# Kernel tuning notes

Measured on AMD Instinct MI355X. Metric: run time of the kernel, lower is better.

Reference implementation:

```python
import jax, jax.numpy as jnp
from jax import lax
import numpy as np

INPUT_SIZE = 1
HIDDEN = 64
OUTPUT = 12
B, S = 2048, 512


def setup_inputs() -> dict:
    key = jax.random.key(0)
    ks = jax.random.split(key, 12)
    bound = 1.0 / np.sqrt(HIDDEN)
    u = lambda k, shape: jax.random.uniform(k, shape, jnp.float32, -bound, bound)
    return {
        "x": jax.random.normal(ks[0], (B, S, INPUT_SIZE), jnp.float32),
        # layer 0 (PyTorch gate order: i, f, g, o stacked along dim 0)
        "w_ih0": u(ks[1], (4 * HIDDEN, INPUT_SIZE)),
        "w_hh0": u(ks[2], (4 * HIDDEN, HIDDEN)),
        "b_ih0": u(ks[3], (4 * HIDDEN,)),
        "b_hh0": u(ks[4], (4 * HIDDEN,)),
        # layer 1
        "w_ih1": u(ks[5], (4 * HIDDEN, HIDDEN)),
        "w_hh1": u(ks[6], (4 * HIDDEN, HIDDEN)),
        "b_ih1": u(ks[7], (4 * HIDDEN,)),
        "b_hh1": u(ks[8], (4 * HIDDEN,)),
        # final projection
        "fc_w": u(ks[9], (OUTPUT, HIDDEN)),
        "fc_b": u(ks[10], (OUTPUT,)),
    }


def _lstm_layer(x_sbi, w_ih, w_hh, b_ih, b_hh):
    """x_sbi: [S, B, in]. Returns hidden sequence [S, B, H]."""
    H = w_hh.shape[1]
    # Precompute input projection for all timesteps (batched GEMM):
    xp = jnp.einsum('sbi,gi->sbg', x_sbi, w_ih) + b_ih + b_hh  # [S, B, 4H]

    def step(carry, xp_t):
        h, c = carry
        gates = xp_t + h @ w_hh.T  # [B, 4H]
        i, f, g, o = jnp.split(gates, 4, axis=-1)
        i = jax.nn.sigmoid(i)
        f = jax.nn.sigmoid(f)
        g = jnp.tanh(g)
        o = jax.nn.sigmoid(o)
        c = f * c + i * g
        h = o * jnp.tanh(c)
        return (h, c), h

    b = x_sbi.shape[1]
    h0 = jnp.zeros((b, H), x_sbi.dtype)
    (_, _), hs = lax.scan(step, (h0, h0), xp)
    return hs  # [S, B, H]


def reference(x, w_ih0, w_hh0, b_ih0, b_hh0, w_ih1, w_hh1, b_ih1, b_hh1, fc_w, fc_b):
    x_sbi = jnp.transpose(x, (1, 0, 2))  # [S, B, in]
    h1 = _lstm_layer(x_sbi, w_ih0, w_hh0, b_ih0, b_hh0)  # [S, B, H]
    h2 = _lstm_layer(h1, w_ih1, w_hh1, b_ih1, b_hh1)     # [S, B, H]
    last = h2[-1]                                          # out[:, -1, :]
    return last @ fc_w.T + fc_b                            # [B, OUTPUT]
```

## Files before the change

kernel.cpp:

```cpp
#include <hip/hip_runtime.h>

#define BT    8
#define HID   64
#define SEQ   512
#define NOUT  12
#define XST   514

typedef float  f32x4 __attribute__((ext_vector_type(4)));
typedef _Float16 f16x8 __attribute__((ext_vector_type(8)));
typedef unsigned int   u32;
typedef unsigned short u16;

union FW { f16x8 v; u32 w[4]; uint4 q; };

__device__ __forceinline__ float rcpf(float x) { return __builtin_amdgcn_rcpf(x); }
__device__ __forceinline__ float e2(float x)   { return __builtin_amdgcn_exp2f(x); }
__device__ __forceinline__ u16 f16b(float a) {
    union { _Float16 f; u16 u; } p; p.f = (_Float16)a; return p.u;
}
__device__ __forceinline__ void split8_f16(const float* src, float scale, f16x8& hi, f16x8& lo) {
    float f[8];
    *(float4*)&f[0] = *(const float4*)src;
    *(float4*)&f[4] = *(const float4*)(src + 4);
    union { f16x8 v; _Float16 h[8]; } H, L;
#pragma unroll
    for (int i = 0; i < 8; ++i) {
        float s = f[i] * scale;
        _Float16 a = (_Float16)s;
        H.h[i] = a;
        L.h[i] = (_Float16)((s - (float)a) * 4096.f);
    }
    hi = H.v; lo = L.v;
}

#define MFMA(A, B, C) __builtin_amdgcn_mfma_f32_16x16x32_f16((A), (B), (C), 0, 0, 0)

__device__ __forceinline__ int swz(int c) { return c ^ (c >> 3); }

__global__ void __launch_bounds__(1024)
lstm2_fused(
    const float* __restrict__ x,
    const float* __restrict__ w_ih0,
    const float* __restrict__ w_hh0,
    const float* __restrict__ b_ih0,
    const float* __restrict__ b_hh0,
    const float* __restrict__ w_ih1,
    const float* __restrict__ w_hh1,
    const float* __restrict__ b_ih1,
    const float* __restrict__ b_hh1,
    const float* __restrict__ fc_w,
    const float* __restrict__ fc_b,
    float* __restrict__ out)
{
    __shared__ float xs[BT][XST];
    __shared__ u32   hf[2048];
    __shared__ float h1last[BT][HID + 4];

    const int tid  = threadIdx.x;
    const int wid  = tid >> 6;
    const int lane = tid & 63;
    const int n    = lane & 15;
    const int qg   = lane >> 4;
    const int b0   = blockIdx.x * BT;

    const float L2E  = 1.44269504088896340736f;
    const float TL2E = 2.f * L2E;

    const int ag   = n & 3;
    const int arow = ag * 64 + 4 * wid + (n >> 2);
    const float asc = (ag == 2) ? TL2E : L2E;
    f16x8 A0h[2], A0l[2], AIh[2], AIl[2], AHh[2], AHl[2];
#pragma unroll
    for (int kt = 0; kt < 2; ++kt) {
        split8_f16(&w_hh0[arow * HID + 32*kt + 8*qg], asc, A0h[kt], A0l[kt]);
        split8_f16(&w_ih1[arow * HID + 32*kt + 8*qg], asc, AIh[kt], AIl[kt]);
        split8_f16(&w_hh1[arow * HID + 32*kt + 8*qg], asc, AHh[kt], AHl[kt]);
    }

    const int ly = (n >> 3) & 1;
    const int bb = n & 7;
    const int uo = 4 * wid + qg;

    float bias0v[4], bias1v[4], wihL[4];
#pragma unroll
    for (int r = 0; r < 4; ++r) {
        const int row = 64 * r + uo;
        const float sc = (r == 2) ? TL2E : L2E;
        bias0v[r] = (b_ih0[row] + b_hh0[row]) * sc;
        bias1v[r] = (b_ih1[row] + b_hh1[row]) * sc;
        wihL[r]   = (ly == 0) ? w_ih0[row] * sc : 0.f;
    }

    const int rb   = swz(lane) << 2;
    const int ktw  = uo >> 5;
    const int qgc  = (uo & 31) >> 3;
    const int wb16 = (ly << 10) + (ktw << 9) + (swz(qgc * 16 + bb) << 3) + (uo & 7);
    const char* hfB = (const char*)hf + rb * 4;
    u16*        hwB = (u16*)hf + wb16;

    for (int i = tid; i < BT * SEQ; i += 1024) {
        int b = i >> 9, t = i & (SEQ - 1);
        xs[b][t] = x[(size_t)(b0 + b) * SEQ + t];
    }
    if (tid < BT) xs[tid][SEQ] = x[(size_t)(b0 + tid) * SEQ + (SEQ - 1)];
    for (int i = tid; i < 2048; i += 1024) hf[i] = 0u;
    float c = 0.f, h = 0.f;
    __syncthreads();

    if (ly == 0) {
        float xv = xs[bb][0];
        float ig = rcpf(1.f + e2(-fmaf(xv, wihL[0], bias0v[0])));
        float gg = fmaf(-2.f, rcpf(1.f + e2(fmaf(xv, wihL[2], bias0v[2]))), 1.f);
        float og = rcpf(1.f + e2(-fmaf(xv, wihL[3], bias0v[3])));
        c = ig * gg;
        h = og * fmaf(-2.f, rcpf(1.f + e2(c * TL2E)), 1.f);
        hwB[0] = f16b(h);
    }
    __syncthreads();

    const float S = 1.f / 4096.f;
    const float* xp = &xs[bb][1];

#define STEP(CUR, NXT, XV)                                                     \
    {                                                                          \
        const float xv = (XV);                                                 \
        FW B00, B01, B10, B11;                                                 \
        B00.q = *(const uint4*)(hfB + (CUR)*4096 + 0);                         \
        B01.q = *(const uint4*)(hfB + (CUR)*4096 + 1024);                      \
        B10.q = *(const uint4*)(hfB + (CUR)*4096 + 2048);                      \
        B11.q = *(const uint4*)(hfB + (CUR)*4096 + 3072);                      \
        f32x4 z4 = {0.f, 0.f, 0.f, 0.f};                                       \
        f32x4 a0H = {bias0v[0], bias0v[1], bias0v[2], bias0v[3]};              \
        f32x4 a1H = {bias1v[0], bias1v[1], bias1v[2], bias1v[3]};              \
        f32x4 a0L = z4, a1L = z4;                                              \
        a0H = MFMA(A0h[0], B00.v, a0H);  a0L = MFMA(A0l[0], B00.v, a0L);       \
        a1H = MFMA(AIh[0], B00.v, a1H);  a1L = MFMA(AIl[0], B00.v, a1L);       \
        a1H = MFMA(AHh[0], B10.v, a1H);  a1L = MFMA(AHl[0], B10.v, a1L);       \
        a0H = MFMA(A0h[1], B01.v, a0H);  a0L = MFMA(A0l[1], B01.v, a0L);       \
        a1H = MFMA(AIh[1], B01.v, a1H);  a1L = MFMA(AIl[1], B01.v, a1L);       \
        a1H = MFMA(AHh[1], B11.v, a1H);  a1L = MFMA(AHl[1], B11.v, a1L);       \
        f32x4 acc0, acc1, accS;                                                \
        _Pragma("unroll")                                                      \
        for (int i = 0; i < 4; ++i) {                                          \
            acc0[i] = fmaf(a0L[i], S, a0H[i]);                                 \
            acc1[i] = fmaf(a1L[i], S, a1H[i]);                                 \
        }                                                                      \
        _Pragma("unroll")                                                      \
        for (int i = 0; i < 4; ++i) {                                          \
            float s = __int_as_float(__builtin_amdgcn_mov_dpp(                 \
                          __float_as_int(acc1[i]), 0x118, 0xF, 0xF, true));    \
            accS[i] = ly ? s : acc0[i];                                        \
        }                                                                      \
        float ig = rcpf(1.f + e2(-fmaf(xv, wihL[0], accS[0])));                \
        float fg = rcpf(1.f + e2(-fmaf(xv, wihL[1], accS[1])));                \
        float gg = fmaf(-2.f, rcpf(1.f + e2(fmaf(xv, wihL[2], accS[2]))), 1.f);\
        float og = rcpf(1.f + e2(-fmaf(xv, wihL[3], accS[3])));                \
        c = fg * c + ig * gg;                                                  \
        h = og * fmaf(-2.f, rcpf(1.f + e2(c * TL2E)), 1.f);                    \
        hwB[(NXT) * 2048] = f16b(h);                                           \
        __syncthreads();                                                       \
    }

    for (int t2 = 0; t2 < SEQ; t2 += 2) {
        STEP(0, 1, xp[0]);
        STEP(1, 0, xp[1]);
        xp += 2;
    }
#undef STEP

    if (ly) h1last[bb][uo] = h;
    __syncthreads();

    if (tid < BT * NOUT) {
        int b = tid / NOUT, o = tid % NOUT;
        float acc = fc_b[o];
#pragma unroll
        for (int j = 0; j < HID; ++j)
            acc = fmaf(fc_w[o * HID + j], h1last[b][j], acc);
        out[(size_t)(b0 + b) * NOUT + o] = acc;
    }
}

extern "C" void kernel_launch(void* const* d_in, const int* in_sizes, int n_in,
                              void* d_out, int out_size, void* d_ws, size_t ws_size,
                              hipStream_t stream) {
    const float* x     = (const float*)d_in[0];
    const float* w_ih0 = (const float*)d_in[1];
    const float* w_hh0 = (const float*)d_in[2];
    const float* b_ih0 = (const float*)d_in[3];
    const float* b_hh0 = (const float*)d_in[4];
    const float* w_ih1 = (const float*)d_in[5];
    const float* w_hh1 = (const float*)d_in[6];
    const float* b_ih1 = (const float*)d_in[7];
    const float* b_hh1 = (const float*)d_in[8];
    const float* fc_w  = (const float*)d_in[9];
    const float* fc_b  = (const float*)d_in[10];

    const int B = in_sizes[0] / SEQ;
    dim3 grid(B / BT);
    lstm2_fused<<<grid, 1024, 0, stream>>>(x, w_ih0, w_hh0, b_ih0, b_hh0,
                                           w_ih1, w_hh1, b_ih1, b_hh1,
                                           fc_w, fc_b, (float*)d_out);
}
```

Before: 405.9 us.

## Drop hi/lo f16 weight split and repartition to 4-batch, 512-thread blocks

Result: slower. 428.0 us (+5.4%).

```diff
diff --git a/kernel.cpp b/kernel.cpp
--- a/kernel.cpp
+++ b/kernel.cpp
@@ -1,6 +1,6 @@
 #include <hip/hip_runtime.h>
 
-#define BT    8
+#define BT    4
 #define HID   64
 #define SEQ   512
 #define NOUT  12
@@ -18,26 +18,25 @@
 __device__ __forceinline__ u16 f16b(float a) {
     union { _Float16 f; u16 u; } p; p.f = (_Float16)a; return p.u;
 }
-__device__ __forceinline__ void split8_f16(const float* src, float scale, f16x8& hi, f16x8& lo) {
+__device__ __forceinline__ f16x8 f16row(const float* src, float scale) {
     float f[8];
     *(float4*)&f[0] = *(const float4*)src;
     *(float4*)&f[4] = *(const float4*)(src + 4);
-    union { f16x8 v; _Float16 h[8]; } H, L;
-#pragma unroll
-    for (int i = 0; i < 8; ++i) {
-        float s = f[i] * scale;
-        _Float16 a = (_Float16)s;
-        H.h[i] = a;
-        L.h[i] = (_Float16)((s - (float)a) * 4096.f);
-    }
-    hi = H.v; lo = L.v;
+    union { f16x8 v; _Float16 h[8]; } H;
+#pragma unroll
+    for (int i = 0; i < 8; ++i) H.h[i] = (_Float16)(f[i] * scale);
+    return H.v;
 }
 
 #define MFMA(A, B, C) __builtin_amdgcn_mfma_f32_16x16x32_f16((A), (B), (C), 0, 0, 0)
 
 __device__ __forceinline__ int swz(int c) { return c ^ (c >> 3); }
-
-__global__ void __launch_bounds__(1024)
+template <int CTL>
+__device__ __forceinline__ float dppf(float v) {
+    return __int_as_float(__builtin_amdgcn_mov_dpp(__float_as_int(v), CTL, 0xF, 0xF, true));
+}
+
+__global__ void __launch_bounds__(512, 4)
 lstm2_fused(
     const float* __restrict__ x,
     const float* __restrict__ w_ih0,
@@ -57,7 +56,7 @@
     __shared__ float h1last[BT][HID + 4];
 
     const int tid  = threadIdx.x;
-    const int wid  = tid >> 6;
+    const int w    = tid >> 6;
     const int lane = tid & 63;
     const int n    = lane & 15;
     const int qg   = lane >> 4;
@@ -66,90 +65,99 @@
     const float L2E  = 1.44269504088896340736f;
     const float TL2E = 2.f * L2E;
 
-    const int ag   = n & 3;
-    const int arow = ag * 64 + 4 * wid + (n >> 2);
-    const float asc = (ag == 2) ? TL2E : L2E;
-    f16x8 A0h[2], A0l[2], AIh[2], AIl[2], AHh[2], AHl[2];
+    const int gA    = n & 3;
+    const int arowA = gA * 64 + 8 * w + (n >> 2);
+    const int arowB = arowA + 4;
+    const float asc = (gA == 2) ? TL2E : L2E;
+    f16x8 A0[2][2], AI[2][2], AH[2][2];
 #pragma unroll
     for (int kt = 0; kt < 2; ++kt) {
-        split8_f16(&w_hh0[arow * HID + 32*kt + 8*qg], asc, A0h[kt], A0l[kt]);
-        split8_f16(&w_ih1[arow * HID + 32*kt + 8*qg], asc, AIh[kt], AIl[kt]);
-        split8_f16(&w_hh1[arow * HID + 32*kt + 8*qg], asc, AHh[kt], AHl[kt]);
-    }
-
-    const int ly = (n >> 3) & 1;
-    const int bb = n & 7;
-    const int uo = 4 * wid + qg;
-
-    float bias0v[4], bias1v[4], wihL[4];
+        A0[0][kt] = f16row(&w_hh0[arowA * HID + 32*kt + 8*qg], asc);
+        A0[1][kt] = f16row(&w_hh0[arowB * HID + 32*kt + 8*qg], asc);
+        AI[0][kt] = f16row(&w_ih1[arowA * HID + 32*kt + 8*qg], asc);
+        AI[1][kt] = f16row(&w_ih1[arowB * HID + 32*kt + 8*qg], asc);
+        AH[0][kt] = f16row(&w_hh1[arowA * HID + 32*kt + 8*qg], asc);
+        AH[1][kt] = f16row(&w_hh1[arowB * HID + 32*kt + 8*qg], asc);
+    }
+
+    const int ua = 8 * w + qg, ub = ua + 4;
+    f32x4 bA0, bB0, bA1, bB1;
 #pragma unroll
     for (int r = 0; r < 4; ++r) {
-        const int row = 64 * r + uo;
         const float sc = (r == 2) ? TL2E : L2E;
-        bias0v[r] = (b_ih0[row] + b_hh0[row]) * sc;
-        bias1v[r] = (b_ih1[row] + b_hh1[row]) * sc;
-        wihL[r]   = (ly == 0) ? w_ih0[row] * sc : 0.f;
+        bA0[r] = (b_ih0[64*r + ua] + b_hh0[64*r + ua]) * sc;
+        bB0[r] = (b_ih0[64*r + ub] + b_hh0[64*r + ub]) * sc;
+        bA1[r] = (b_ih1[64*r + ua] + b_hh1[64*r + ua]) * sc;
+        bB1[r] = (b_ih1[64*r + ub] + b_hh1[64*r + ub]) * sc;
+    }
+
+    const int  ly = n >> 3;
+    const int  bb = n & 3;
+    const int  uo = 8 * w + 4 * ((n >> 2) & 1) + qg;
+    const bool m1 = (n >> 2) & 1;
+    float wihL[4], bie0[4];
+#pragma unroll
+    for (int r = 0; r < 4; ++r) {
+        const float sc = (r == 2) ? TL2E : L2E;
+        wihL[r] = (ly == 0) ? w_ih0[64*r + uo] * sc : 0.f;
+        bie0[r] = m1 ? bB0[r] : bA0[r];
     }
 
     const int rb   = swz(lane) << 2;
-    const int ktw  = uo >> 5;
-    const int qgc  = (uo & 31) >> 3;
-    const int wb16 = (ly << 10) + (ktw << 9) + (swz(qgc * 16 + bb) << 3) + (uo & 7);
+    const int wb16 = (ly << 10) + ((uo >> 5) << 9)
+                   + (swz(((uo & 31) >> 3) * 16 + bb) << 3) + (uo & 7);
     const char* hfB = (const char*)hf + rb * 4;
     u16*        hwB = (u16*)hf + wb16;
 
-    for (int i = tid; i < BT * SEQ; i += 1024) {
+    for (int i = tid; i < BT * SEQ; i += 512) {
         int b = i >> 9, t = i & (SEQ - 1);
         xs[b][t] = x[(size_t)(b0 + b) * SEQ + t];
     }
     if (tid < BT) xs[tid][SEQ] = x[(size_t)(b0 + tid) * SEQ + (SEQ - 1)];
-    for (int i = tid; i < 2048; i += 1024) hf[i] = 0u;
+    for (int i = tid; i < 2048; i += 512) hf[i] = 0u;
     float c = 0.f, h = 0.f;
     __syncthreads();
 
     if (ly == 0) {
         float xv = xs[bb][0];
-        float ig = rcpf(1.f + e2(-fmaf(xv, wihL[0], bias0v[0])));
-        float gg = fmaf(-2.f, rcpf(1.f + e2(fmaf(xv, wihL[2], bias0v[2]))), 1.f);
-        float og = rcpf(1.f + e2(-fmaf(xv, wihL[3], bias0v[3])));
+        float ig = rcpf(1.f + e2(-fmaf(xv, wihL[0], bie0[0])));
+        float gg = fmaf(-2.f, rcpf(1.f + e2(fmaf(xv, wihL[2], bie0[2]))), 1.f);
+        float og = rcpf(1.f + e2(-fmaf(xv, wihL[3], bie0[3])));
         c = ig * gg;
         h = og * fmaf(-2.f, rcpf(1.f + e2(c * TL2E)), 1.f);
         hwB[0] = f16b(h);
     }
     __syncthreads();
 
-    const float S = 1.f / 4096.f;
-    const float* xp = &xs[bb][1];
-
-#define STEP(CUR, NXT, XV)                                                     \
+#define STEP(CUR, NXT)                                                         \
     {                                                                          \
-        const float xv = (XV);                                                 \
+        const float xv = *xp2++;                                               \
         FW B00, B01, B10, B11;                                                 \
         B00.q = *(const uint4*)(hfB + (CUR)*4096 + 0);                         \
         B01.q = *(const uint4*)(hfB + (CUR)*4096 + 1024);                      \
         B10.q = *(const uint4*)(hfB + (CUR)*4096 + 2048);                      \
         B11.q = *(const uint4*)(hfB + (CUR)*4096 + 3072);                      \
-        f32x4 z4 = {0.f, 0.f, 0.f, 0.f};                                       \
-        f32x4 a0H = {bias0v[0], bias0v[1], bias0v[2], bias0v[3]};              \
-        f32x4 a1H = {bias1v[0], bias1v[1], bias1v[2], bias1v[3]};              \
-        f32x4 a0L = z4, a1L = z4;                                              \
-        a0H = MFMA(A0h[0], B00.v, a0H);  a0L = MFMA(A0l[0], B00.v, a0L);       \
-        a1H = MFMA(AIh[0], B00.v, a1H);  a1L = MFMA(AIl[0], B00.v, a1L);       \
-        a1H = MFMA(AHh[0], B10.v, a1H);  a1L = MFMA(AHl[0], B10.v, a1L);       \
-        a0H = MFMA(A0h[1], B01.v, a0H);  a0L = MFMA(A0l[1], B01.v, a0L);       \
-        a1H = MFMA(AIh[1], B01.v, a1H);  a1L = MFMA(AIl[1], B01.v, a1L);       \
-        a1H = MFMA(AHh[1], B11.v, a1H);  a1L = MFMA(AHl[1], B11.v, a1L);       \
-        f32x4 acc0, acc1, accS;                                                \
+        f32x4 a0A = MFMA(A0[0][0], B00.v, bA0);                                \
+        f32x4 a0B = MFMA(A0[1][0], B00.v, bB0);                                \
+        f32x4 a1A = MFMA(AI[0][0], B00.v, bA1);                                \
+        f32x4 a1B = MFMA(AI[1][0], B00.v, bB1);                                \
+        a0A = MFMA(A0[0][1], B01.v, a0A);                                      \
+        a0B = MFMA(A0[1][1], B01.v, a0B);                                      \
+        a1A = MFMA(AH[0][0], B10.v, a1A);                                      \
+        a1B = MFMA(AH[1][0], B10.v, a1B);                                      \
+        a1A = MFMA(AI[0][1], B01.v, a1A);                                      \
+        a1B = MFMA(AI[1][1], B01.v, a1B);                                      \
+        a1A = MFMA(AH[0][1], B11.v, a1A);                                      \
+        a1B = MFMA(AH[1][1], B11.v, a1B);                                      \
+        f32x4 accS;                                                            \
         _Pragma("unroll")                                                      \
         for (int i = 0; i < 4; ++i) {                                          \
-            acc0[i] = fmaf(a0L[i], S, a0H[i]);                                 \
-            acc1[i] = fmaf(a1L[i], S, a1H[i]);                                 \
-        }                                                                      \
-        _Pragma("unroll")                                                      \
-        for (int i = 0; i < 4; ++i) {                                          \
-            float s = __int_as_float(__builtin_amdgcn_mov_dpp(                 \
-                          __float_as_int(acc1[i]), 0x118, 0xF, 0xF, true));    \
-            accS[i] = ly ? s : acc0[i];                                        \
+            float s4  = dppf<0x114>(a0B[i]);                   \
+            float s8  = dppf<0x118>(a1A[i]);                   \
+            float s12 = dppf<0x11C>(a1B[i]);                   \
+            float v0 = m1 ? s4  : a0A[i];                                      \
+            float v1 = m1 ? s12 : s8;                                          \
+            accS[i] = ly ? v1 : v0;                                            \
         }                                                                      \
         float ig = rcpf(1.f + e2(-fmaf(xv, wihL[0], accS[0])));                \
         float fg = rcpf(1.f + e2(-fmaf(xv, wihL[1], accS[1])));                \
@@ -161,10 +169,12 @@
         __syncthreads();                                                       \
     }
 
-    for (int t2 = 0; t2 < SEQ; t2 += 2) {
-        STEP(0, 1, xp[0]);
-        STEP(1, 0, xp[1]);
-        xp += 2;
+    {
+        const float* xp2 = &xs[bb][1];
+        for (int t2 = 0; t2 < SEQ; t2 += 2) {
+            STEP(0, 1);
+            STEP(1, 0);
+        }
     }
 #undef STEP
 
@@ -198,7 +208,7 @@
 
     const int B = in_sizes[0] / SEQ;
     dim3 grid(B / BT);
-    lstm2_fused<<<grid, 1024, 0, stream>>>(x, w_ih0, w_hh0, b_ih0, b_hh0,
-                                           w_ih1, w_hh1, b_ih1, b_hh1,
-                                           fc_w, fc_b, (float*)d_out);
-}
+    lstm2_fused<<<grid, 512, 0, stream>>>(x, w_ih0, w_hh0, b_ih0, b_hh0,
+                                          w_ih1, w_hh1, b_ih1, b_hh1,
+                                          fc_w, fc_b, (float*)d_out);
+}
```
